# Kernel tuning notes

Measured on AMD Instinct MI355X. Metric: run time of the kernel, lower is better.

Reference implementation:

```python
import jax, jax.numpy as jnp
import numpy as np

EPS = 1e-5

def layer_norm(x, g, b):
    mu = jnp.mean(x, axis=-1, keepdims=True)
    var = jnp.var(x, axis=-1, keepdims=True)
    return (x - mu) * jax.lax.rsqrt(var + EPS) * g + b

def setup_inputs() -> dict:
    key = jax.random.key(0)
    N, C, K = 50000, 64, 16
    ks = jax.random.split(key, 16)
    def lin(k, fan_in, fan_out):
        bound = 1.0 / np.sqrt(fan_in)
        kw, kb = jax.random.split(k)
        W = jax.random.uniform(kw, (fan_in, fan_out), minval=-bound, maxval=bound, dtype=jnp.float32)
        b = jax.random.uniform(kb, (fan_out,), minval=-bound, maxval=bound, dtype=jnp.float32)
        return W, b
    wq, bq = lin(ks[0], C, C)
    wk, bk = lin(ks[1], C, C)
    wv, bv = lin(ks[2], C, C)
    wp, bp = lin(ks[3], 3, C)
    wg1, bg1 = lin(ks[4], C, C)
    wg2, bg2 = lin(ks[5], C, C)
    wo, bo = lin(ks[6], C, C)
    return {
        'points': jax.random.normal(ks[7], (N, 3), dtype=jnp.float32),
        'features': jax.random.normal(ks[8], (N, C), dtype=jnp.float32),
        'neighbor_idx': jax.random.randint(ks[9], (N, K), 0, N, dtype=jnp.int32),
        'wq': wq, 'bq': bq, 'wk': wk, 'bk': bk, 'wv': wv, 'bv': bv,
        'wp': wp, 'bp': bp, 'gp': jnp.ones((C,), jnp.float32), 'betap': jnp.zeros((C,), jnp.float32),
        'wg1': wg1, 'bg1': bg1, 'gg': jnp.ones((C,), jnp.float32), 'betag': jnp.zeros((C,), jnp.float32),
        'wg2': wg2, 'bg2': bg2, 'wo': wo, 'bo': bo,
    }

def reference(points, features, neighbor_idx, wq, bq, wk, bk, wv, bv,
              wp, bp, gp, betap, wg1, bg1, gg, betag, wg2, bg2, wo, bo):
    # residual_proj is Identity since in_planes == out_planes
    residual = features
    q = features @ wq + bq                      # (N, C)
    k = features @ wk + bk
    v = features @ wv + bv
    gpts = points[neighbor_idx]                 # (N, K, 3)
    gk = k[neighbor_idx]                        # (N, K, C)
    gv = v[neighbor_idx]
    rel = gpts - points[:, None, :]             # (N, K, 3)
    p = jax.nn.relu(layer_norm(rel @ wp + bp, gp, betap))  # (N, K, C)
    attn_in = q[:, None, :] - gk + p            # (N, K, C)
    h = jax.nn.relu(layer_norm(attn_in @ wg1 + bg1, gg, betag))
    w = h @ wg2 + bg2                           # (N, K, C)
    w = jax.nn.softmax(w, axis=1)               # softmax over neighbor axis
    out = jnp.sum((gv + p) * w, axis=1)         # (N, C)
    return out @ wo + bo + residual
```

## Files before the change

kernel.cpp:

```cpp
#include <hip/hip_runtime.h>

typedef __attribute__((ext_vector_type(8))) short bfrag8;
typedef __attribute__((ext_vector_type(4))) short bfrag4;
typedef __attribute__((ext_vector_type(4))) float f32x4;

#if defined(__has_builtin)
#if __has_builtin(__builtin_amdgcn_cvt_pk_bf16_f32)
#define HAVE_PK_BF16 1
#endif
#endif

__device__ __forceinline__ float bf2f(unsigned short h){
  unsigned u = ((unsigned)h) << 16;
  return __builtin_bit_cast(float, u);
}
__device__ __forceinline__ unsigned short f2bf(float f){
  unsigned u = __builtin_bit_cast(unsigned, f);
  u = u + 0x7FFFu + ((u >> 16) & 1u);
  return (unsigned short)(u >> 16);
}
__device__ __forceinline__ unsigned pk2bf(float a, float b){
#ifdef HAVE_PK_BF16
  typedef __attribute__((ext_vector_type(2))) __bf16 bf16x2_t;
  bf16x2_t r = __builtin_amdgcn_cvt_pk_bf16_f32(a, b);
  return __builtin_bit_cast(unsigned, r);
#else
  return (unsigned)f2bf(a) | ((unsigned)f2bf(b) << 16);
#endif
}
__device__ __forceinline__ bfrag8 gload8(const unsigned short* p){
  int4 v = *(const int4*)p;
  return __builtin_bit_cast(bfrag8, v);
}
__device__ __forceinline__ bfrag8 lds_load8(const unsigned short* p){
  bfrag4 lo = *(const bfrag4*)p;
  bfrag4 hi = *(const bfrag4*)(p + 4);
  bfrag8 r;
#pragma unroll
  for (int j = 0; j < 4; j++){ r[j] = lo[j]; r[4+j] = hi[j]; }
  return r;
}
__device__ __forceinline__ f32x4 mfma16(bfrag8 a, bfrag8 b, f32x4 c){
  return __builtin_amdgcn_mfma_f32_16x16x32_bf16(a, b, c, 0, 0, 0);
}

__device__ __forceinline__ float ldf(const void* p, size_t i, int f32){
  return f32 ? ((const float*)p)[i] : bf2f(((const unsigned short*)p)[i]);
}
__device__ __forceinline__ unsigned short ldbf(const void* p, size_t i, int f32){
  return f32 ? f2bf(((const float*)p)[i]) : ((const unsigned short*)p)[i];
}
__device__ __forceinline__ bfrag8 load8bf(const void* p, size_t base, int f32){
  if (f32){
    const float* f = (const float*)p + base;
    float4 x = *(const float4*)f;
    float4 y = *(const float4*)(f + 4);
    bfrag8 r;
    r[0]=(short)f2bf(x.x); r[1]=(short)f2bf(x.y); r[2]=(short)f2bf(x.z); r[3]=(short)f2bf(x.w);
    r[4]=(short)f2bf(y.x); r[5]=(short)f2bf(y.y); r[6]=(short)f2bf(y.z); r[7]=(short)f2bf(y.w);
    return r;
  }
  return gload8((const unsigned short*)p + base);
}

template<int CTRL>
__device__ __forceinline__ float dpp_add(float x){
  int xi = __builtin_bit_cast(int, x);
  int yi = __builtin_amdgcn_update_dpp(0, xi, CTRL, 0xF, 0xF, true);
  return x + __builtin_bit_cast(float, yi);
}
__device__ __forceinline__ float row16_sum(float x){
  x = dpp_add<0xB1>(x);
  x = dpp_add<0x4E>(x);
  x = dpp_add<0x141>(x);
  x = dpp_add<0x140>(x);
  return x;
}
__device__ __forceinline__ float xgrp_sum(float x){
  x += __shfl_xor(x, 16, 64);
  x += __shfl_xor(x, 32, 64);
  return x;
}
__device__ __forceinline__ int wave_isum(int x){
#pragma unroll
  for (int s = 1; s < 64; s <<= 1) x += __shfl_xor(x, s, 64);
  return x;
}

struct Ptrs { const void* p[21]; int n[21]; };
struct PrepPtrs { const void* w[6]; const void* wp; const void* b[11]; };

__global__ void detect_kernel(Ptrs ptrs, int* flags){
  const int lane = threadIdx.x & 63;
  const int wid = blockIdx.x * 4 + (threadIdx.x >> 6);
  if (wid >= 21) return;
  if (wid == 2){ if (lane == 0) flags[2] = 0; return; }

  const unsigned short* p = (const unsigned short*)ptrs.p[wid];
  int m = ptrs.n[wid]; if (m > 128) m = 128;
  int insane = 0, evenZero = 0, evenCnt = 0, oddNZ = 0, oddCnt = 0;
#pragma unroll
  for (int s = 0; s < 2; s++){
    int i = lane + s*64;
    if (i < m){
      unsigned short h = p[i];
      int e = (h >> 7) & 0xFF;
      bool z = (h & 0x7FFF) == 0;
      if (!z && (e == 0xFF || e < 90 || e > 140)) insane++;
      if (i & 1){ oddCnt++;  if (!z) oddNZ++; }
      else      { evenCnt++; if (z)  evenZero++; }
    }
  }
  insane = wave_isum(insane);
  evenZero = wave_isum(evenZero); evenCnt = wave_isum(evenCnt);
  oddNZ = wave_isum(oddNZ);       oddCnt = wave_isum(oddCnt);
  if (lane == 0){
    int f = 0;
    if (insane > 0) f = 1;
    else if (evenZero * 4 >= evenCnt * 3 && oddNZ * 4 >= oddCnt * 3) f = 1;
    flags[wid] = f;
  }
}

__global__ void prep_kernel(PrepPtrs pp, const int* __restrict__ flags,
                            unsigned short* __restrict__ wfrag,
                            unsigned short* __restrict__ wp_bf,
                            float* __restrict__ biases)
{
  const int gid = blockIdx.x * 256 + threadIdx.x;
  const int gstride = gridDim.x * 256;
  const int wflag[6] = {3,5,7,13,17,19};
  for (int idx = gid; idx < 6*4096; idx += gstride){
    int m = idx >> 12;
    int r = idx & 4095;
    int j = r & 7;
    int lane = (r >> 3) & 63;
    int kt = r >> 9;
    int ks = kt >> 2, t = kt & 3;
    int o = lane >> 4, rl = lane & 15;
    int src = (ks*32 + o*8 + j)*64 + t*16 + rl;
    wfrag[idx] = ldbf(pp.w[m], src, flags[wflag[m]]);
  }
  if (blockIdx.x == 0){
    for (int i = threadIdx.x; i < 192; i += 256) wp_bf[i] = ldbf(pp.wp, i, flags[9]);
    const int bflag[11] = {4,6,8,10,11,12,14,15,16,18,20};
    for (int i = threadIdx.x; i < 11*64; i += 256){
      int m = i >> 6;
      biases[i] = ldf(pp.b[m], i & 63, flags[bflag[m]]);
    }
  }
}

__global__ __launch_bounds__(256, 2)
void qkv_kernel(const void* __restrict__ feat,
                const unsigned short* __restrict__ wfrag,
                const float* __restrict__ biases,
                unsigned short* __restrict__ q_ws, unsigned short* __restrict__ k_ws,
                unsigned short* __restrict__ v_ws, const int* __restrict__ flags, int N)
{
  const int F_feat = flags[1];
  const int lane = threadIdx.x & 63;
  const int wave = threadIdx.x >> 6;
  const int o = lane >> 4, rl = lane & 15;

  bfrag8 wqf[2][4], wkf[2][4], wvf[2][4];
#pragma unroll
  for (int ks = 0; ks < 2; ks++)
#pragma unroll
    for (int t = 0; t < 4; t++){
      int off = ((ks*4 + t)*64 + lane)*8;
      wqf[ks][t] = gload8(wfrag + off);
      wkf[ks][t] = gload8(wfrag + 4096 + off);
      wvf[ks][t] = gload8(wfrag + 8192 + off);
    }
  float bqC[4], bkC[4], bvC[4];
#pragma unroll
  for (int t = 0; t < 4; t++){
    bqC[t] = biases[0*64 + t*16 + rl];
    bkC[t] = biases[1*64 + t*16 + rl];
    bvC[t] = biases[2*64 + t*16 + rl];
  }

  const int ntiles = (N + 15) >> 4;
  for (int tile = blockIdx.x*4 + wave; tile < ntiles; tile += gridDim.x*4){
    const int n0 = tile * 16;
    int ar = n0 + rl; if (ar >= N) ar = N - 1;
    bfrag8 a[2];
#pragma unroll
    for (int ks = 0; ks < 2; ks++) a[ks] = load8bf(feat, (size_t)ar*64 + ks*32 + o*8, F_feat);

    f32x4 zq[4], zk[4], zv[4];
#pragma unroll
    for (int t = 0; t < 4; t++){
      f32x4 aq = {0.f,0.f,0.f,0.f}, ak = {0.f,0.f,0.f,0.f}, av = {0.f,0.f,0.f,0.f};
#pragma unroll
      for (int ks = 0; ks < 2; ks++){
        aq = mfma16(a[ks], wqf[ks][t], aq);
        ak = mfma16(a[ks], wkf[ks][t], ak);
        av = mfma16(a[ks], wvf[ks][t], av);
      }
      zq[t] = aq; zk[t] = ak; zv[t] = av;
    }
#pragma unroll
    for (int q = 0; q < 4; q++){
      size_t row = n0 + o*4 + q;
      if ((int)row < N){
        size_t e = row*64 + 4*rl;
        uint2 u;
        u.x = pk2bf(zq[0][q]+bqC[0], zq[1][q]+bqC[1]);
        u.y = pk2bf(zq[2][q]+bqC[2], zq[3][q]+bqC[3]);
        *(uint2*)(q_ws + e) = u;
        u.x = pk2bf(zk[0][q]+bkC[0], zk[1][q]+bkC[1]);
        u.y = pk2bf(zk[2][q]+bkC[2], zk[3][q]+bkC[3]);
        *(uint2*)(k_ws + e) = u;
        u.x = pk2bf(zv[0][q]+bvC[0], zv[1][q]+bvC[1]);
        u.y = pk2bf(zv[2][q]+bvC[2], zv[3][q]+bvC[3]);
        *(uint2*)(v_ws + e) = u;
      }
    }
  }
}

__global__ __launch_bounds__(256, 2)
void pt_kernel(const void* __restrict__ points,
               const void* __restrict__ feat,
               const int* __restrict__ nidx,
               const unsigned short* __restrict__ q_ws,
               const unsigned short* __restrict__ k_ws,
               const unsigned short* __restrict__ v_ws,
               const unsigned short* __restrict__ wfrag,
               const unsigned short* __restrict__ wp_bf,
               const float* __restrict__ biases,
               const int* __restrict__ flags, void* __restrict__ out, int N)
{
  __shared__ unsigned short xbuf[4][16][68];
  __shared__ unsigned short ybuf[4][64];

  const int F_pts = flags[0], F_feat = flags[1];
  const int lane = threadIdx.x & 63;
  const int wave = threadIdx.x >> 6;
  const int o = lane >> 4, rl = lane & 15;

  bfrag8 wg1f[2][4], wg2f[2][4], wof[2][4];
#pragma unroll
  for (int ks = 0; ks < 2; ks++)
#pragma unroll
    for (int t = 0; t < 4; t++){
      int off = ((ks*4 + t)*64 + lane)*8;
      wg1f[ks][t] = gload8(wfrag + 3*4096 + off);
      wg2f[ks][t] = gload8(wfrag + 4*4096 + off);
      wof[ks][t]  = gload8(wfrag + 5*4096 + off);
    }
  bfrag8 wpf[4];
#pragma unroll
  for (int t = 0; t < 4; t++){
    bfrag8 a = {0,0,0,0,0,0,0,0};
    if (o == 0){
#pragma unroll
      for (int j = 0; j < 3; j++) a[j] = (short)wp_bf[j*64 + t*16 + rl];
    }
    wpf[t] = a;
  }
  float bpC[4], gpC[4], bePC[4], bg1C[4], ggC[4], beGC[4], bg2C[4], boC[4];
#pragma unroll
  for (int t = 0; t < 4; t++){
    int c = t*16 + rl;
    bpC[t]  = biases[3*64 + c];  gpC[t]  = biases[4*64 + c];  bePC[t] = biases[5*64 + c];
    bg1C[t] = biases[6*64 + c];  ggC[t]  = biases[7*64 + c];  beGC[t] = biases[8*64 + c];
    bg2C[t] = biases[9*64 + c];  boC[t]  = biases[10*64 + c];
  }

  const int wstride = gridDim.x * 4;
  for (int n = blockIdx.x*4 + wave; n < N; n += wstride){
    const int jr = nidx[n*16 + rl];
    int jq[4];
#pragma unroll
    for (int q = 0; q < 4; q++) jq[q] = nidx[n*16 + o*4 + q];

    float qC[4], gkC[4][4], gvC[4][4];
    {
      ushort4 uq = *(const ushort4*)(q_ws + (size_t)n*64 + 4*rl);
      qC[0] = bf2f(uq.x); qC[1] = bf2f(uq.y); qC[2] = bf2f(uq.z); qC[3] = bf2f(uq.w);
    }
#pragma unroll
    for (int q = 0; q < 4; q++){
      size_t e = (size_t)jq[q]*64 + 4*rl;
      ushort4 uk = *(const ushort4*)(k_ws + e);
      ushort4 uv = *(const ushort4*)(v_ws + e);
      gkC[0][q] = bf2f(uk.x); gkC[1][q] = bf2f(uk.y); gkC[2][q] = bf2f(uk.z); gkC[3][q] = bf2f(uk.w);
      gvC[0][q] = bf2f(uv.x); gvC[1][q] = bf2f(uv.y); gvC[2][q] = bf2f(uv.z); gvC[3][q] = bf2f(uv.w);
    }
    const float res = ldf(feat, (size_t)n*64 + lane, F_feat);
    float rel[3];
#pragma unroll
    for (int d = 0; d < 3; d++)
      rel[d] = ldf(points, (size_t)jr*3 + d, F_pts) - ldf(points, (size_t)n*3 + d, F_pts);

    bfrag8 ap = {0,0,0,0,0,0,0,0};
    if (o == 0){
#pragma unroll
      for (int d = 0; d < 3; d++) ap[d] = (short)f2bf(rel[d]);
    }
    f32x4 pacc[4];
#pragma unroll
    for (int t = 0; t < 4; t++){
      f32x4 z = {0.f,0.f,0.f,0.f};
      pacc[t] = mfma16(ap, wpf[t], z);
    }
    float p_val[4][4];
#pragma unroll
    for (int q = 0; q < 4; q++){
      float xv[4]; float s = 0.f, s2 = 0.f;
#pragma unroll
      for (int t = 0; t < 4; t++){ xv[t] = pacc[t][q] + bpC[t]; s += xv[t]; s2 += xv[t]*xv[t]; }
      s = row16_sum(s); s2 = row16_sum(s2);
      float mu = s * (1.f/64.f);
      float var = s2 * (1.f/64.f) - mu*mu;
      float rs = rsqrtf(var + 1e-5f);
#pragma unroll
      for (int t = 0; t < 4; t++){
        float a = rs * gpC[t];
        p_val[t][q] = fmaxf(xv[t]*a + (bePC[t] - mu*a), 0.f);
      }
    }

#pragma unroll
    for (int q = 0; q < 4; q++){
      float a0 = qC[0] - gkC[0][q] + p_val[0][q];
      float a1 = qC[1] - gkC[1][q] + p_val[1][q];
      float a2 = qC[2] - gkC[2][q] + p_val[2][q];
      float a3 = qC[3] - gkC[3][q] + p_val[3][q];
      unsigned u01 = pk2bf(a0, a1), u23 = pk2bf(a2, a3);
      int r = o*4 + q;
      xbuf[wave][r][0*16 + rl] = (unsigned short)u01;
      xbuf[wave][r][1*16 + rl] = (unsigned short)(u01 >> 16);
      xbuf[wave][r][2*16 + rl] = (unsigned short)u23;
      xbuf[wave][r][3*16 + rl] = (unsigned short)(u23 >> 16);
    }
    f32x4 hacc[4] = {{0.f,0.f,0.f,0.f},{0.f,0.f,0.f,0.f},{0.f,0.f,0.f,0.f},{0.f,0.f,0.f,0.f}};
#pragma unroll
    for (int ks = 0; ks < 2; ks++){
      bfrag8 af = lds_load8(&xbuf[wave][rl][ks*32 + o*8]);
#pragma unroll
      for (int t = 0; t < 4; t++) hacc[t] = mfma16(af, wg1f[ks][t], hacc[t]);
    }

    float h_val[4][4];
#pragma unroll
    for (int q = 0; q < 4; q++){
      float xv[4]; float s = 0.f, s2 = 0.f;
#pragma unroll
      for (int t = 0; t < 4; t++){ xv[t] = hacc[t][q] + bg1C[t]; s += xv[t]; s2 += xv[t]*xv[t]; }
      s = row16_sum(s); s2 = row16_sum(s2);
      float mu = s * (1.f/64.f);
      float var = s2 * (1.f/64.f) - mu*mu;
      float rs = rsqrtf(var + 1e-5f);
#pragma unroll
      for (int t = 0; t < 4; t++){
        float a = rs * ggC[t];
        h_val[t][q] = fmaxf(xv[t]*a + (beGC[t] - mu*a), 0.f);
      }
      unsigned u01 = pk2bf(h_val[0][q], h_val[1][q]);
      unsigned u23 = pk2bf(h_val[2][q], h_val[3][q]);
      int r = o*4 + q;
      xbuf[wave][r][0*16 + rl] = (unsigned short)u01;
      xbuf[wave][r][1*16 + rl] = (unsigned short)(u01 >> 16);
      xbuf[wave][r][2*16 + rl] = (unsigned short)u23;
      xbuf[wave][r][3*16 + rl] = (unsigned short)(u23 >> 16);
    }
    f32x4 wacc[4] = {{0.f,0.f,0.f,0.f},{0.f,0.f,0.f,0.f},{0.f,0.f,0.f,0.f},{0.f,0.f,0.f,0.f}};
#pragma unroll
    for (int ks = 0; ks < 2; ks++){
      bfrag8 hf = lds_load8(&xbuf[wave][rl][ks*32 + o*8]);
#pragma unroll
      for (int t = 0; t < 4; t++) wacc[t] = mfma16(hf, wg2f[ks][t], wacc[t]);
    }

    float y[4];
#pragma unroll
    for (int t = 0; t < 4; t++){
      float se = 0.f, z = 0.f;
#pragma unroll
      for (int q = 0; q < 4; q++){
        float e = __expf(wacc[t][q] + bg2C[t]);
        se += e;
        z  += e * (gvC[t][q] + p_val[t][q]);
      }
      se = xgrp_sum(se); z = xgrp_sum(z);
      y[t] = z * __builtin_amdgcn_rcpf(se);
    }

    if (o == 0){
      unsigned u01 = pk2bf(y[0], y[1]), u23 = pk2bf(y[2], y[3]);
      ybuf[wave][0*16 + rl] = (unsigned short)u01;
      ybuf[wave][1*16 + rl] = (unsigned short)(u01 >> 16);
      ybuf[wave][2*16 + rl] = (unsigned short)u23;
      ybuf[wave][3*16 + rl] = (unsigned short)(u23 >> 16);
    }
    f32x4 oacc[4] = {{0.f,0.f,0.f,0.f},{0.f,0.f,0.f,0.f},{0.f,0.f,0.f,0.f},{0.f,0.f,0.f,0.f}};
#pragma unroll
    for (int ks = 0; ks < 2; ks++){
      bfrag8 yf = lds_load8(&ybuf[wave][ks*32 + o*8]);
#pragma unroll
      for (int t = 0; t < 4; t++) oacc[t] = mfma16(yf, wof[ks][t], oacc[t]);
    }

    float ov = 0.f;
#pragma unroll
    for (int t = 0; t < 4; t++) if (o == t) ov = oacc[t][0] + boC[t];
    float outv = ov + res;
    if (F_feat) ((float*)out)[(size_t)n*64 + lane] = outv;
    else ((unsigned short*)out)[(size_t)n*64 + lane] = f2bf(outv);
  }
}

extern "C" void kernel_launch(void* const* d_in, const int* in_sizes, int n_in,
                              void* d_out, int out_size, void* d_ws, size_t ws_size,
                              hipStream_t stream)
{
  const int N = in_sizes[1] / 64;

  unsigned short* q_ws = (unsigned short*)d_ws;
  unsigned short* k_ws = q_ws + (size_t)N * 64;
  unsigned short* v_ws = k_ws + (size_t)N * 64;
  char* base = (char*)d_ws + (size_t)3 * N * 64 * sizeof(unsigned short);
  int*            flags  = (int*)base;
  unsigned short* wfrag  = (unsigned short*)(base + 256);
  unsigned short* wp_bf  = (unsigned short*)(base + 256 + 49152);
  float*          biases = (float*)(base + 256 + 49152 + 512);

  Ptrs ptrs;
  for (int i = 0; i < 21; i++){ ptrs.p[i] = d_in[i]; ptrs.n[i] = in_sizes[i]; }
  PrepPtrs pp;
  pp.w[0] = d_in[3];  pp.w[1] = d_in[5];  pp.w[2] = d_in[7];
  pp.w[3] = d_in[13]; pp.w[4] = d_in[17]; pp.w[5] = d_in[19];
  pp.wp = d_in[9];
  pp.b[0] = d_in[4];  pp.b[1] = d_in[6];  pp.b[2] = d_in[8];  pp.b[3] = d_in[10];
  pp.b[4] = d_in[11]; pp.b[5] = d_in[12]; pp.b[6] = d_in[14]; pp.b[7] = d_in[15];
  pp.b[8] = d_in[16]; pp.b[9] = d_in[18]; pp.b[10] = d_in[20];

  detect_kernel<<<6, 256, 0, stream>>>(ptrs, flags);
  prep_kernel<<<32, 256, 0, stream>>>(pp, flags, wfrag, wp_bf, biases);
  qkv_kernel<<<512, 256, 0, stream>>>(d_in[1], wfrag, biases, q_ws, k_ws, v_ws, flags, N);
  pt_kernel<<<1024, 256, 0, stream>>>(d_in[0], d_in[1], (const int*)d_in[2], q_ws, k_ws, v_ws,
                                      wfrag, wp_bf, biases, flags, d_out, N);
}
```

Baseline: 214.7 us.

## Compute LayerNorm means via extra MFMA with row-summed weights, vectorize LDS stores

Precomputes the row sums of wp and wg1 (and the sums of their biases) in the prep kernel, so each LayerNorm mean comes from one extra MFMA instead of a cross-lane DPP reduction. The K dimension of the wg1/wg2/wo fragments is permuted so that the packed 4-element LDS stores become a single uint2 write per lane, replacing four scalar short stores. Gathered K/V values stay packed bf16 until they are used, which is meant to lower register pressure. In exchange it adds MFMA work, grows the workspace layout, and computes the mean from bf16-rounded summed weights, which slightly changes numerics.

```diff
diff --git a/kernel.cpp b/kernel.cpp
--- a/kernel.cpp
+++ b/kernel.cpp
@@ -87,6 +87,11 @@
   return x;
 }
 
+__device__ __host__ __forceinline__ int permC(int p){ return (p >> 2) + 16 * (p & 3); }
+
+#define WS1_OFF 24576
+#define WPS_OFF 25600
+
 struct Ptrs { const void* p[21]; int n[21]; };
 struct PrepPtrs { const void* w[6]; const void* wp; const void* b[11]; };
 
@@ -127,7 +132,8 @@
                             unsigned short* __restrict__ wp_bf,
                             float* __restrict__ biases)
 {
-  const int gid = blockIdx.x * 256 + threadIdx.x;
+  const int tid = threadIdx.x;
+  const int gid = blockIdx.x * 256 + tid;
   const int gstride = gridDim.x * 256;
   const int wflag[6] = {3,5,7,13,17,19};
   for (int idx = gid; idx < 6*4096; idx += gstride){
@@ -138,13 +144,61 @@
     int kt = r >> 9;
     int ks = kt >> 2, t = kt & 3;
     int o = lane >> 4, rl = lane & 15;
-    int src = (ks*32 + o*8 + j)*64 + t*16 + rl;
+    int kslot = ks*32 + o*8 + j;
+    int k_log = (m >= 3) ? permC(kslot) : kslot;
+    int src = k_log*64 + t*16 + rl;
     wfrag[idx] = ldbf(pp.w[m], src, flags[wflag[m]]);
   }
   if (blockIdx.x == 0){
-    for (int i = threadIdx.x; i < 192; i += 256) wp_bf[i] = ldbf(pp.wp, i, flags[9]);
+    __shared__ float part[64][4];
+    __shared__ float ws1sh[64];
+    __shared__ float wpssh[3];
+    {
+      int c = tid >> 2, q = tid & 3;
+      float s = 0.f;
+#pragma unroll
+      for (int u = 0; u < 16; u++) s += ldf(pp.w[3], c*64 + q*16 + u, flags[13]);
+      part[c][q] = s;
+    }
+    __syncthreads();
+    if (tid < 64) ws1sh[tid] = part[tid][0] + part[tid][1] + part[tid][2] + part[tid][3];
+    __syncthreads();
+    if (tid < 12){
+      int k = tid >> 2, q = tid & 3;
+      float s = 0.f;
+#pragma unroll
+      for (int u = 0; u < 16; u++) s += ldf(pp.wp, k*64 + q*16 + u, flags[9]);
+      part[k][q] = s;
+    }
+    __syncthreads();
+    if (tid < 3) wpssh[tid] = part[tid][0] + part[tid][1] + part[tid][2] + part[tid][3];
+    if (tid == 4){
+      float s = 0.f;
+      for (int i = 0; i < 64; i++) s += ldf(pp.b[3], i, flags[10]);
+      biases[704] = s;
+    }
+    if (tid == 5){
+      float s = 0.f;
+      for (int i = 0; i < 64; i++) s += ldf(pp.b[6], i, flags[14]);
+      biases[705] = s;
+    }
+    __syncthreads();
+    for (int i = tid; i < 1024; i += 256){
+      int j = i & 7, lane = (i >> 3) & 63, ks = i >> 9;
+      int o = lane >> 4;
+      int c = permC(ks*32 + o*8 + j);
+      wfrag[WS1_OFF + i] = f2bf(ws1sh[c]);
+    }
+    for (int i = tid; i < 512; i += 256){
+      int j = i & 7, lane = i >> 3;
+      int o = lane >> 4;
+      unsigned short v = 0;
+      if (o == 0 && j < 3) v = f2bf(wpssh[j]);
+      wfrag[WPS_OFF + i] = v;
+    }
+    for (int i = tid; i < 192; i += 256) wp_bf[i] = ldbf(pp.wp, i, flags[9]);
     const int bflag[11] = {4,6,8,10,11,12,14,15,16,18,20};
-    for (int i = threadIdx.x; i < 11*64; i += 256){
+    for (int i = tid; i < 11*64; i += 256){
       int m = i >> 6;
       biases[i] = ldf(pp.b[m], i & 63, flags[bflag[m]]);
     }
@@ -241,16 +295,20 @@
   const int wave = threadIdx.x >> 6;
   const int o = lane >> 4, rl = lane & 15;
 
-  bfrag8 wg1f[2][4], wg2f[2][4], wof[2][4];
+  bfrag8 wg1f[2][4], wg2f[2][4], wof[2][4], ws1f[2], wpsf;
 #pragma unroll
   for (int ks = 0; ks < 2; ks++)
 #pragma unroll
     for (int t = 0; t < 4; t++){
       int off = ((ks*4 + t)*64 + lane)*8;
-      wg1f[ks][t] = gload8(wfrag + 3*4096 + off);
-      wg2f[ks][t] = gload8(wfrag + 4*4096 + off);
-      wof[ks][t]  = gload8(wfrag + 5*4096 + off);
-    }
+      wg1f[ks][t] = gload8(wfrag + 12288 + off);
+      wg2f[ks][t] = gload8(wfrag + 16384 + off);
+      wof[ks][t]  = gload8(wfrag + 20480 + off);
+    }
+#pragma unroll
+  for (int ks = 0; ks < 2; ks++) ws1f[ks] = gload8(wfrag + WS1_OFF + (ks*64 + lane)*8);
+  wpsf = gload8(wfrag + WPS_OFF + lane*8);
+
   bfrag8 wpf[4];
 #pragma unroll
   for (int t = 0; t < 4; t++){
@@ -269,26 +327,22 @@
     bg1C[t] = biases[6*64 + c];  ggC[t]  = biases[7*64 + c];  beGC[t] = biases[8*64 + c];
     bg2C[t] = biases[9*64 + c];  boC[t]  = biases[10*64 + c];
   }
+  const float sum_bp  = biases[704];
+  const float sum_bg1 = biases[705];
 
   const int wstride = gridDim.x * 4;
   for (int n = blockIdx.x*4 + wave; n < N; n += wstride){
+    int4 jqv = *(const int4*)(nidx + n*16 + o*4);
     const int jr = nidx[n*16 + rl];
-    int jq[4];
-#pragma unroll
-    for (int q = 0; q < 4; q++) jq[q] = nidx[n*16 + o*4 + q];
-
-    float qC[4], gkC[4][4], gvC[4][4];
-    {
-      ushort4 uq = *(const ushort4*)(q_ws + (size_t)n*64 + 4*rl);
-      qC[0] = bf2f(uq.x); qC[1] = bf2f(uq.y); qC[2] = bf2f(uq.z); qC[3] = bf2f(uq.w);
-    }
+    int jq[4] = {jqv.x, jqv.y, jqv.z, jqv.w};
+
+    ushort4 uq = *(const ushort4*)(q_ws + (size_t)n*64 + 4*rl);
+    ushort4 gk_pk[4], gv_pk[4];
 #pragma unroll
     for (int q = 0; q < 4; q++){
       size_t e = (size_t)jq[q]*64 + 4*rl;
-      ushort4 uk = *(const ushort4*)(k_ws + e);
-      ushort4 uv = *(const ushort4*)(v_ws + e);
-      gkC[0][q] = bf2f(uk.x); gkC[1][q] = bf2f(uk.y); gkC[2][q] = bf2f(uk.z); gkC[3][q] = bf2f(uk.w);
-      gvC[0][q] = bf2f(uv.x); gvC[1][q] = bf2f(uv.y); gvC[2][q] = bf2f(uv.z); gvC[3][q] = bf2f(uv.w);
+      gk_pk[q] = *(const ushort4*)(k_ws + e);
+      gv_pk[q] = *(const ushort4*)(v_ws + e);
     }
     const float res = ldf(feat, (size_t)n*64 + lane, F_feat);
     float rel[3];
@@ -307,14 +361,17 @@
       f32x4 z = {0.f,0.f,0.f,0.f};
       pacc[t] = mfma16(ap, wpf[t], z);
     }
+    f32x4 zz = {0.f,0.f,0.f,0.f};
+    f32x4 pacc_s = mfma16(ap, wpsf, zz);
+
     float p_val[4][4];
 #pragma unroll
     for (int q = 0; q < 4; q++){
-      float xv[4]; float s = 0.f, s2 = 0.f;
-#pragma unroll
-      for (int t = 0; t < 4; t++){ xv[t] = pacc[t][q] + bpC[t]; s += xv[t]; s2 += xv[t]*xv[t]; }
-      s = row16_sum(s); s2 = row16_sum(s2);
-      float mu = s * (1.f/64.f);
+      float xv[4]; float s2 = 0.f;
+#pragma unroll
+      for (int t = 0; t < 4; t++){ xv[t] = pacc[t][q] + bpC[t]; s2 += xv[t]*xv[t]; }
+      s2 = row16_sum(s2);
+      float mu = (pacc_s[q] + sum_bp) * (1.f/64.f);
       float var = s2 * (1.f/64.f) - mu*mu;
       float rs = rsqrtf(var + 1e-5f);
 #pragma unroll
@@ -324,56 +381,56 @@
       }
     }
 
+    float qC[4];
+    qC[0] = bf2f(uq.x); qC[1] = bf2f(uq.y); qC[2] = bf2f(uq.z); qC[3] = bf2f(uq.w);
 #pragma unroll
     for (int q = 0; q < 4; q++){
-      float a0 = qC[0] - gkC[0][q] + p_val[0][q];
-      float a1 = qC[1] - gkC[1][q] + p_val[1][q];
-      float a2 = qC[2] - gkC[2][q] + p_val[2][q];
-      float a3 = qC[3] - gkC[3][q] + p_val[3][q];
-      unsigned u01 = pk2bf(a0, a1), u23 = pk2bf(a2, a3);
-      int r = o*4 + q;
-      xbuf[wave][r][0*16 + rl] = (unsigned short)u01;
-      xbuf[wave][r][1*16 + rl] = (unsigned short)(u01 >> 16);
-      xbuf[wave][r][2*16 + rl] = (unsigned short)u23;
-      xbuf[wave][r][3*16 + rl] = (unsigned short)(u23 >> 16);
-    }
+      float a0 = qC[0] - bf2f(gk_pk[q].x) + p_val[0][q];
+      float a1 = qC[1] - bf2f(gk_pk[q].y) + p_val[1][q];
+      float a2 = qC[2] - bf2f(gk_pk[q].z) + p_val[2][q];
+      float a3 = qC[3] - bf2f(gk_pk[q].w) + p_val[3][q];
+      uint2 w2; w2.x = pk2bf(a0, a1); w2.y = pk2bf(a2, a3);
+      *(uint2*)&xbuf[wave][o*4 + q][4*rl] = w2;
+    }
+    bfrag8 af0 = lds_load8(&xbuf[wave][rl][o*8]);
+    bfrag8 af1 = lds_load8(&xbuf[wave][rl][32 + o*8]);
+
     f32x4 hacc[4] = {{0.f,0.f,0.f,0.f},{0.f,0.f,0.f,0.f},{0.f,0.f,0.f,0.f},{0.f,0.f,0.f,0.f}};
 #pragma unroll
-    for (int ks = 0; ks < 2; ks++){
-      bfrag8 af = lds_load8(&xbuf[wave][rl][ks*32 + o*8]);
-#pragma unroll
-      for (int t = 0; t < 4; t++) hacc[t] = mfma16(af, wg1f[ks][t], hacc[t]);
-    }
-
-    float h_val[4][4];
+    for (int t = 0; t < 4; t++){
+      hacc[t] = mfma16(af0, wg1f[0][t], hacc[t]);
+      hacc[t] = mfma16(af1, wg1f[1][t], hacc[t]);
+    }
+    f32x4 sacc = {0.f,0.f,0.f,0.f};
+    sacc = mfma16(af0, ws1f[0], sacc);
+    sacc = mfma16(af1, ws1f[1], sacc);
+
 #pragma unroll
     for (int q = 0; q < 4; q++){
-      float xv[4]; float s = 0.f, s2 = 0.f;
-#pragma unroll
-      for (int t = 0; t < 4; t++){ xv[t] = hacc[t][q] + bg1C[t]; s += xv[t]; s2 += xv[t]*xv[t]; }
-      s = row16_sum(s); s2 = row16_sum(s2);
-      float mu = s * (1.f/64.f);
+      float xv[4]; float s2 = 0.f;
+#pragma unroll
+      for (int t = 0; t < 4; t++){ xv[t] = hacc[t][q] + bg1C[t]; s2 += xv[t]*xv[t]; }
+      s2 = row16_sum(s2);
+      float mu = (sacc[q] + sum_bg1) * (1.f/64.f);
       float var = s2 * (1.f/64.f) - mu*mu;
       float rs = rsqrtf(var + 1e-5f);
-#pragma unroll
-      for (int t = 0; t < 4; t++){
-        float a = rs * ggC[t];
-        h_val[t][q] = fmaxf(xv[t]*a + (beGC[t] - mu*a), 0.f);
+      float h0, h1, h2, h3;
+      {
+        float a0 = rs * ggC[0]; h0 = fmaxf(xv[0]*a0 + (beGC[0] - mu*a0), 0.f);
+        float a1 = rs * ggC[1]; h1 = fmaxf(xv[1]*a1 + (beGC[1] - mu*a1), 0.f);
+        float a2 = rs * ggC[2]; h2 = fmaxf(xv[2]*a2 + (beGC[2] - mu*a2), 0.f);
+        float a3 = rs * ggC[3]; h3 = fmaxf(xv[3]*a3 + (beGC[3] - mu*a3), 0.f);
       }
-      unsigned u01 = pk2bf(h_val[0][q], h_val[1][q]);
-      unsigned u23 = pk2bf(h_val[2][q], h_val[3][q]);
-      int r = o*4 + q;
-      xbuf[wave][r][0*16 + rl] = (unsigned short)u01;
-      xbuf[wave][r][1*16 + rl] = (unsigned short)(u01 >> 16);
-      xbuf[wave][r][2*16 + rl] = (unsigned short)u23;
-      xbuf[wave][r][3*16 + rl] = (unsigned short)(u23 >> 16);
-    }
+      uint2 w2; w2.x = pk2bf(h0, h1); w2.y = pk2bf(h2, h3);
+      *(uint2*)&xbuf[wave][o*4 + q][4*rl] = w2;
+    }
+    bfrag8 hf0 = lds_load8(&xbuf[wave][rl][o*8]);
+    bfrag8 hf1 = lds_load8(&xbuf[wave][rl][32 + o*8]);
     f32x4 wacc[4] = {{0.f,0.f,0.f,0.f},{0.f,0.f,0.f,0.f},{0.f,0.f,0.f,0.f},{0.f,0.f,0.f,0.f}};
 #pragma unroll
-    for (int ks = 0; ks < 2; ks++){
-      bfrag8 hf = lds_load8(&xbuf[wave][rl][ks*32 + o*8]);
-#pragma unroll
-      for (int t = 0; t < 4; t++) wacc[t] = mfma16(hf, wg2f[ks][t], wacc[t]);
+    for (int t = 0; t < 4; t++){
+      wacc[t] = mfma16(hf0, wg2f[0][t], wacc[t]);
+      wacc[t] = mfma16(hf1, wg2f[1][t], wacc[t]);
     }
 
     float y[4];
@@ -383,26 +440,26 @@
 #pragma unroll
       for (int q = 0; q < 4; q++){
         float e = __expf(wacc[t][q] + bg2C[t]);
+        float gv = (t==0) ? bf2f(gv_pk[q].x) : (t==1) ? bf2f(gv_pk[q].y)
+                 : (t==2) ? bf2f(gv_pk[q].z) : bf2f(gv_pk[q].w);
         se += e;
-        z  += e * (gvC[t][q] + p_val[t][q]);
+        z  += e * (gv + p_val[t][q]);
       }
       se = xgrp_sum(se); z = xgrp_sum(z);
       y[t] = z * __builtin_amdgcn_rcpf(se);
     }
 
     if (o == 0){
-      unsigned u01 = pk2bf(y[0], y[1]), u23 = pk2bf(y[2], y[3]);
-      ybuf[wave][0*16 + rl] = (unsigned short)u01;
-      ybuf[wave][1*16 + rl] = (unsigned short)(u01 >> 16);
-      ybuf[wave][2*16 + rl] = (unsigned short)u23;
-      ybuf[wave][3*16 + rl] = (unsigned short)(u23 >> 16);
-    }
+      uint2 w2; w2.x = pk2bf(y[0], y[1]); w2.y = pk2bf(y[2], y[3]);
+      *(uint2*)&ybuf[wave][4*rl] = w2;
+    }
+    bfrag8 yf0 = lds_load8(&ybuf[wave][o*8]);
+    bfrag8 yf1 = lds_load8(&ybuf[wave][32 + o*8]);
     f32x4 oacc[4] = {{0.f,0.f,0.f,0.f},{0.f,0.f,0.f,0.f},{0.f,0.f,0.f,0.f},{0.f,0.f,0.f,0.f}};
 #pragma unroll
-    for (int ks = 0; ks < 2; ks++){
-      bfrag8 yf = lds_load8(&ybuf[wave][ks*32 + o*8]);
-#pragma unroll
-      for (int t = 0; t < 4; t++) oacc[t] = mfma16(yf, wof[ks][t], oacc[t]);
+    for (int t = 0; t < 4; t++){
+      oacc[t] = mfma16(yf0, wof[0][t], oacc[t]);
+      oacc[t] = mfma16(yf1, wof[1][t], oacc[t]);
     }
 
     float ov = 0.f;
@@ -426,8 +483,8 @@
   char* base = (char*)d_ws + (size_t)3 * N * 64 * sizeof(unsigned short);
   int*            flags  = (int*)base;
   unsigned short* wfrag  = (unsigned short*)(base + 256);
-  unsigned short* wp_bf  = (unsigned short*)(base + 256 + 49152);
-  float*          biases = (float*)(base + 256 + 49152 + 512);
+  unsigned short* wp_bf  = (unsigned short*)(base + 256 + 53248);
+  float*          biases = (float*)(base + 256 + 53248 + 512);
 
   Ptrs ptrs;
   for (int i = 0; i < 21; i++){ ptrs.p[i] = d_in[i]; ptrs.n[i] = in_sizes[i]; }
```

Result: slower. 227.1 us (+5.8%).
